# Performance work log

Measured on AMD Instinct MI355X. Metric: run time of the kernel, lower is better.

## Reference

```python
import math
import jax, jax.numpy as jnp
import numpy as np

D_MODEL = 768
N_HEADS = 12


def setup_inputs() -> dict:
    key = jax.random.key(0)
    kx, kw, kb = jax.random.split(key, 3)
    x = jax.random.normal(kx, (2, 2048, D_MODEL), dtype=jnp.float32)
    # nn.Linear(D, 3D): weight [3D, D], bias [3D]; init ~ U(-1/sqrt(D), 1/sqrt(D))
    bound = 1.0 / math.sqrt(D_MODEL)
    W_kqv = jax.random.uniform(kw, (3 * D_MODEL, D_MODEL), dtype=jnp.float32, minval=-bound, maxval=bound)
    b_kqv = jax.random.uniform(kb, (3 * D_MODEL,), dtype=jnp.float32, minval=-bound, maxval=bound)
    return {"x": x, "W_kqv": W_kqv, "b_kqv": b_kqv}


def reference(x, W_kqv, b_kqv):
    N, C, D = x.shape
    H = N_HEADS
    hd = D // H
    z = jnp.einsum('ncd,ed->nce', x, W_kqv) + b_kqv  # [N, C, 3D]
    # order in source: k first, then q, then v
    k = z[:, :, :D].reshape(N, C, H, hd).transpose(0, 2, 1, 3)       # [N,H,C,hd]
    q = z[:, :, D:2 * D].reshape(N, C, H, hd).transpose(0, 2, 1, 3)
    v = z[:, :, 2 * D:].reshape(N, C, H, hd).transpose(0, 2, 1, 3)
    # NOTE: faithful to source: scale by sqrt(D) (full model dim), not sqrt(head_dim)
    scores = jnp.einsum('nhqd,nhkd->nhqk', q, k) / math.sqrt(D)
    causal = jnp.tril(jnp.ones((C, C), dtype=bool))
    scores = jnp.where(causal, scores, -jnp.inf)
    attn = jax.nn.softmax(scores, axis=-1)
    out = jnp.einsum('nhqk,nhkd->nhqd', attn, v)  # [N,H,C,hd]
    return out.transpose(0, 2, 1, 3).reshape(N, C, D)
```

## Files before the change

kernel.cpp:

```cpp
#include <hip/hip_runtime.h>
#include <stdint.h>

#define D_MODEL 768
#define E3      2304
#define NCTX    2048
#define NH      12
#define HD      64
#define MROWS   4096
#define NHTOT   24

typedef __attribute__((ext_vector_type(8))) short short8;
typedef __attribute__((ext_vector_type(4))) short bf16x4;
typedef __attribute__((ext_vector_type(4))) float f32x4;

typedef __attribute__((address_space(3))) uint32_t lds_u32;
typedef __attribute__((address_space(1))) uint32_t glob_u32;

__device__ __forceinline__ void async_copy16(const void* g, void* l) {
    __builtin_amdgcn_global_load_lds((const glob_u32*)(uintptr_t)g,
                                     (lds_u32*)(uint32_t)(uintptr_t)l, 16, 0, 0);
}

__device__ __forceinline__ unsigned short f2bf(float f) {
    uint32_t u = __builtin_bit_cast(uint32_t, f);
    u += 0x7fffu + ((u >> 16) & 1u);
    return (unsigned short)(u >> 16);
}

__device__ __forceinline__ float fast_exp2(float x) {
#if __has_builtin(__builtin_amdgcn_exp2f)
    return __builtin_amdgcn_exp2f(x);
#else
    return __expf(x * 0.6931471805599453f);
#endif
}

#if __has_builtin(__builtin_amdgcn_mfma_f32_16x16x16bf16_1k)
#define HAVE_MFMA16 1
#else
#define HAVE_MFMA16 0
#endif

__global__ void cast_bf16_kernel(const float* __restrict__ in, unsigned short* __restrict__ out) {
    int i = blockIdx.x * blockDim.x + threadIdx.x;
    float4 v = ((const float4*)in)[i];
    ushort4 o;
    o.x = f2bf(v.x); o.y = f2bf(v.y); o.z = f2bf(v.z); o.w = f2bf(v.w);
    ((ushort4*)out)[i] = o;
}

__global__ __launch_bounds__(256) void qkv_gemm(const unsigned short* __restrict__ A,
                                                const unsigned short* __restrict__ B,
                                                const float* __restrict__ bias,
                                                unsigned short* __restrict__ Zq,
                                                unsigned short* __restrict__ Kb,
                                                unsigned short* __restrict__ Vb) {
    __shared__ __attribute__((aligned(16))) unsigned short sA[128 * 64];
    __shared__ __attribute__((aligned(16))) unsigned short sB[128 * 64];

    const int tid  = threadIdx.x;
    const int wave = tid >> 6;
    const int lane = tid & 63;
    const int quad = lane >> 4;
    const int l15  = lane & 15;
    const int wm   = (wave >> 1) << 6;
    const int wn   = (wave & 1) << 6;
    const int row0 = blockIdx.y * 128;
    const int col0 = blockIdx.x * 128;

    const int srow   = lane >> 3;
    const int schunk = (lane & 7) * 8;

    f32x4 acc[4][4] = {};

    for (int k0 = 0; k0 < D_MODEL; k0 += 64) {
        __syncthreads();
#pragma unroll
        for (int c = 0; c < 4; ++c) {
            const int rbase = wave * 32 + c * 8;
            async_copy16(A + (size_t)(row0 + rbase + srow) * D_MODEL + k0 + schunk, &sA[rbase * 64]);
            async_copy16(B + (size_t)(col0 + rbase + srow) * D_MODEL + k0 + schunk, &sB[rbase * 64]);
        }
        __syncthreads();

#pragma unroll
        for (int ks = 0; ks < 2; ++ks) {
            short8 aF[4], bF[4];
#pragma unroll
            for (int i = 0; i < 4; ++i)
                aF[i] = *(const short8*)&sA[(wm + i * 16 + l15) * 64 + ks * 32 + quad * 8];
#pragma unroll
            for (int i = 0; i < 4; ++i)
                bF[i] = *(const short8*)&sB[(wn + i * 16 + l15) * 64 + ks * 32 + quad * 8];
#pragma unroll
            for (int i = 0; i < 4; ++i)
#pragma unroll
                for (int j = 0; j < 4; ++j)
                    acc[i][j] = __builtin_amdgcn_mfma_f32_16x16x32_bf16(aF[i], bF[j], acc[i][j], 0, 0, 0);
        }
    }

    if (col0 < D_MODEL) {
#pragma unroll
        for (int j = 0; j < 4; ++j) {
            const int col = col0 + wn + j * 16 + l15;
            const float bv = bias[col];
            const int h = col >> 6, d = col & 63;
            const int ks = d >> 5, quadd = (d >> 3) & 3, e = d & 7;
#pragma unroll
            for (int i = 0; i < 4; ++i) {
                const int row = row0 + wm + i * 16 + quad * 4;
                const int n = row >> 11;
                const int key = row & (NCTX - 1);
                const int kb = key >> 6;
                const int ct = i;
                const size_t base = ((size_t)((n * NH + h) * 32 + kb)) * 4096
                                  + (((ks * 4 + ct) * 4 + quadd) * 16) * 8 + e;
#pragma unroll
                for (int r = 0; r < 4; ++r)
                    Kb[base + (size_t)(quad * 4 + r) * 8] = f2bf(acc[i][j][r] + bv);
            }
        }
    } else if (col0 < 2 * D_MODEL) {
        const float zscale = 0.036084391824351615f * 1.4426950408889634f;
#pragma unroll
        for (int j = 0; j < 4; ++j) {
            const int col = col0 - D_MODEL + wn + j * 16 + l15;
            const float bv = bias[col0 + wn + j * 16 + l15];
#pragma unroll
            for (int i = 0; i < 4; ++i) {
                const int row = row0 + wm + i * 16 + quad * 4;
#pragma unroll
                for (int r = 0; r < 4; ++r)
                    Zq[(size_t)(row + r) * D_MODEL + col] = f2bf((acc[i][j][r] + bv) * zscale);
            }
        }
    } else {
#pragma unroll
        for (int j = 0; j < 4; ++j) {
            const int col = col0 + wn + j * 16 + l15;
            const float bv = bias[col];
            const int ch = col - 2 * D_MODEL;
            const int h = ch >> 6, d = ch & 63;
            const int dt = d >> 4, l15d = d & 15;
#pragma unroll
            for (int i = 0; i < 4; ++i) {
                const int row = row0 + wm + i * 16 + quad * 4;
                const int n = row >> 11;
                const int key = row & (NCTX - 1);
                const int kb = key >> 6;
                const int ct = i, quadv = quad;
                ushort4 w4;
                w4.x = f2bf(acc[i][j][0] + bv);
                w4.y = f2bf(acc[i][j][1] + bv);
                w4.z = f2bf(acc[i][j][2] + bv);
                w4.w = f2bf(acc[i][j][3] + bv);
                *(ushort4*)&Vb[((size_t)((n * NH + h) * 32 + kb)) * 4096
                               + (((ct * 4 + dt) * 4 + quadv) * 16 + l15d) * 4] = w4;
            }
        }
    }
}

__global__ __launch_bounds__(256) void attn_kernel(const unsigned short* __restrict__ Zq,
                                                   const unsigned short* __restrict__ Kb,
                                                   const unsigned short* __restrict__ Vb,
                                                   float* __restrict__ out) {
    __shared__ __attribute__((aligned(16))) unsigned short sK[2][4096];
    __shared__ __attribute__((aligned(16))) unsigned short sV[2][4096];
#if !HAVE_MFMA16
    __shared__ __attribute__((aligned(16))) unsigned short sP[4][16 * 72];
#endif

    const int tid  = threadIdx.x;
    const int wave = tid >> 6;
    const int lane = tid & 63;
    const int quad = lane >> 4;
    const int l15  = lane & 15;
    const int b    = blockIdx.x;
    const int t    = (NCTX / 64 - 1) - b / NHTOT;
    const int nh   = b - (b / NHTOT) * NHTOT;
    const int n    = nh / NH;
    const int h    = nh - n * NH;

    const unsigned short* KbP = Kb + (size_t)(nh * 32) * 4096;
    const unsigned short* VbP = Vb + (size_t)(nh * 32) * 4096;

    const unsigned short* Qp = Zq + (size_t)(n * NCTX + t * 64 + wave * 16) * D_MODEL + h * HD;
    short8 qf[2];
#pragma unroll
    for (int ks = 0; ks < 2; ++ks)
        qf[ks] = *(const short8*)&Qp[(size_t)l15 * D_MODEL + ks * 32 + quad * 8];

    f32x4 o[4] = {};
    float lsum = 0.0f;

#pragma unroll
    for (int c = 0; c < 2; ++c) {
        const int off = wave * 1024 + c * 512;
        async_copy16(KbP + off + lane * 8, &sK[0][off]);
        async_copy16(VbP + off + lane * 8, &sV[0][off]);
    }

    for (int kb = 0; kb <= t; ++kb) {
        const int buf = kb & 1;
        __syncthreads();
        if (kb < t) {
#pragma unroll
            for (int c = 0; c < 2; ++c) {
                const int off = wave * 1024 + c * 512;
                async_copy16(KbP + (size_t)(kb + 1) * 4096 + off + lane * 8, &sK[buf ^ 1][off]);
                async_copy16(VbP + (size_t)(kb + 1) * 4096 + off + lane * 8, &sV[buf ^ 1][off]);
            }
        }

        short8 kf[2][4];
#pragma unroll
        for (int ks = 0; ks < 2; ++ks)
#pragma unroll
            for (int ct = 0; ct < 4; ++ct)
                kf[ks][ct] = *(const short8*)&sK[buf][(ks * 4 + ct) * 512 + lane * 8];

        f32x4 s[4] = {};
#pragma unroll
        for (int ct = 0; ct < 4; ++ct) {
            s[ct] = __builtin_amdgcn_mfma_f32_16x16x32_bf16(kf[0][ct], qf[0], s[ct], 0, 0, 0);
            s[ct] = __builtin_amdgcn_mfma_f32_16x16x32_bf16(kf[1][ct], qf[1], s[ct], 0, 0, 0);
        }

        const bool diag = (kb == t);
        const int qg = t * 64 + wave * 16 + l15;
#if HAVE_MFMA16
        bf16x4 pA[4];
#endif
#pragma unroll
        for (int ct = 0; ct < 4; ++ct) {
            float pv[4];
#pragma unroll
            for (int r = 0; r < 4; ++r) {
                const int key = kb * 64 + ct * 16 + quad * 4 + r;
                float sv = s[ct][r];
                if (diag && key > qg) sv = -INFINITY;
                pv[r] = fast_exp2(sv);
                lsum += pv[r];
            }
#if HAVE_MFMA16
            pA[ct][0] = (short)f2bf(pv[0]); pA[ct][1] = (short)f2bf(pv[1]);
            pA[ct][2] = (short)f2bf(pv[2]); pA[ct][3] = (short)f2bf(pv[3]);
#else
            ushort4 w4;
            w4.x = f2bf(pv[0]); w4.y = f2bf(pv[1]); w4.z = f2bf(pv[2]); w4.w = f2bf(pv[3]);
            *(ushort4*)&sP[wave][l15 * 72 + ct * 16 + quad * 4] = w4;
#endif
        }

#if HAVE_MFMA16
#pragma unroll
        for (int ct = 0; ct < 4; ++ct)
#pragma unroll
            for (int dt = 0; dt < 4; ++dt) {
                const bf16x4 vf = *(const bf16x4*)&sV[buf][(ct * 4 + dt) * 256 + lane * 4];
                o[dt] = __builtin_amdgcn_mfma_f32_16x16x16bf16_1k(pA[ct], vf, o[dt], 0, 0, 0);
            }
#else
        const short8 pf0 = *(const short8*)&sP[wave][l15 * 72 + quad * 8];
        const short8 pf1 = *(const short8*)&sP[wave][l15 * 72 + 32 + quad * 8];
#pragma unroll
        for (int dt = 0; dt < 4; ++dt) {
            short8 vf0, vf1;
#pragma unroll
            for (int e = 0; e < 8; ++e) {
                const int k0 = quad * 8 + e;
                const int k1 = 32 + quad * 8 + e;
                vf0[e] = (short)sV[buf][(((k0 >> 4) * 4 + dt) * 4 + ((k0 >> 2) & 3)) * 64 + l15 * 4 + (k0 & 3)];
                vf1[e] = (short)sV[buf][(((k1 >> 4) * 4 + dt) * 4 + ((k1 >> 2) & 3)) * 64 + l15 * 4 + (k1 & 3)];
            }
            o[dt] = __builtin_amdgcn_mfma_f32_16x16x32_bf16(pf0, vf0, o[dt], 0, 0, 0);
            o[dt] = __builtin_amdgcn_mfma_f32_16x16x32_bf16(pf1, vf1, o[dt], 0, 0, 0);
        }
#endif
    }

    float l = lsum;
    l += __shfl_xor(l, 16);
    l += __shfl_xor(l, 32);
    const float linv = 1.0f / l;
#pragma unroll
    for (int r = 0; r < 4; ++r) {
        const float inv = __shfl(linv, quad * 4 + r);
        const size_t row = (size_t)n * NCTX + t * 64 + wave * 16 + quad * 4 + r;
#pragma unroll
        for (int dt = 0; dt < 4; ++dt)
            out[row * D_MODEL + h * HD + dt * 16 + l15] = o[dt][r] * inv;
    }
}

extern "C" void kernel_launch(void* const* d_in, const int* in_sizes, int n_in,
                              void* d_out, int out_size, void* d_ws, size_t ws_size,
                              hipStream_t stream) {
    const float* x = (const float*)d_in[0];
    const float* W = (const float*)d_in[1];
    const float* b = (const float*)d_in[2];
    float* out = (float*)d_out;

    unsigned short* xb = (unsigned short*)d_ws;
    unsigned short* Wb = xb + (size_t)MROWS * D_MODEL;
    unsigned short* Zq = Wb + (size_t)E3 * D_MODEL;
    unsigned short* Kb = Zq + (size_t)MROWS * D_MODEL;
    unsigned short* Vb = Kb + (size_t)NHTOT * 32 * 4096;

    cast_bf16_kernel<<<dim3((MROWS * D_MODEL / 4) / 256), 256, 0, stream>>>(x, xb);
    cast_bf16_kernel<<<dim3((E3 * D_MODEL / 4) / 256), 256, 0, stream>>>(W, Wb);
    qkv_gemm<<<dim3(E3 / 128, MROWS / 128), 256, 0, stream>>>(xb, Wb, b, Zq, Kb, Vb);
    attn_kernel<<<dim3(NHTOT * (NCTX / 64)), 256, 0, stream>>>(Zq, Kb, Vb, out);
}
```

Baseline: 146.7 us.

## Triple-buffer attention K/V loads, remap blocks per XCD, merge cast kernels

The attention kernel moves from double to triple buffering of K/V tiles in LDS. It prefetches two tiles ahead and uses explicit vmcnt waits plus a raw barrier instead of __syncthreads, so loads can overlap more compute. Block indices are remapped so that the heads sharing an XCD stay together, meant to improve L2 reuse of K/V, and MFMA sections get raised wave priority. The two fp32-to-bf16 cast launches are merged into one kernel, saving a launch. The cost is 50% more LDS per block, which may lower occupancy, and a hand-coded vmcnt count that must match the number of outstanding loads.

```diff
diff --git a/kernel.cpp b/kernel.cpp
--- a/kernel.cpp
+++ b/kernel.cpp
@@ -41,12 +41,21 @@
 #define HAVE_MFMA16 0
 #endif
 
-__global__ void cast_bf16_kernel(const float* __restrict__ in, unsigned short* __restrict__ out) {
+__global__ __launch_bounds__(256) void cast2_bf16_kernel(const float* __restrict__ a,
+                                                         unsigned short* __restrict__ oa,
+                                                         int na4,
+                                                         const float* __restrict__ b,
+                                                         unsigned short* __restrict__ ob) {
     int i = blockIdx.x * blockDim.x + threadIdx.x;
-    float4 v = ((const float4*)in)[i];
+    const float4* src;
+    ushort4* dst;
+    int idx;
+    if (i < na4) { src = (const float4*)a; dst = (ushort4*)oa; idx = i; }
+    else         { src = (const float4*)b; dst = (ushort4*)ob; idx = i - na4; }
+    float4 v = src[idx];
     ushort4 o;
     o.x = f2bf(v.x); o.y = f2bf(v.y); o.z = f2bf(v.z); o.w = f2bf(v.w);
-    ((ushort4*)out)[i] = o;
+    dst[idx] = o;
 }
 
 __global__ __launch_bounds__(256) void qkv_gemm(const unsigned short* __restrict__ A,
@@ -166,8 +175,8 @@
                                                    const unsigned short* __restrict__ Kb,
                                                    const unsigned short* __restrict__ Vb,
                                                    float* __restrict__ out) {
-    __shared__ __attribute__((aligned(16))) unsigned short sK[2][4096];
-    __shared__ __attribute__((aligned(16))) unsigned short sV[2][4096];
+    __shared__ __attribute__((aligned(16))) unsigned short sK[3][4096];
+    __shared__ __attribute__((aligned(16))) unsigned short sV[3][4096];
 #if !HAVE_MFMA16
     __shared__ __attribute__((aligned(16))) unsigned short sP[4][16 * 72];
 #endif
@@ -178,8 +187,10 @@
     const int quad = lane >> 4;
     const int l15  = lane & 15;
     const int b    = blockIdx.x;
-    const int t    = (NCTX / 64 - 1) - b / NHTOT;
-    const int nh   = b - (b / NHTOT) * NHTOT;
+    const int xcd  = b & 7;
+    const int ii   = b >> 3;
+    const int t    = 31 - ii / 3;
+    const int nh   = (ii % 3) * 8 + xcd;
     const int n    = nh / NH;
     const int h    = nh - n * NH;
 
@@ -195,23 +206,30 @@
     f32x4 o[4] = {};
     float lsum = 0.0f;
 
-#pragma unroll
-    for (int c = 0; c < 2; ++c) {
-        const int off = wave * 1024 + c * 512;
-        async_copy16(KbP + off + lane * 8, &sK[0][off]);
-        async_copy16(VbP + off + lane * 8, &sV[0][off]);
-    }
-
+#define STAGE(kbi, bufi)                                                          \
+    do {                                                                          \
+        const size_t gof = (size_t)(kbi) * 4096;                                  \
+        _Pragma("unroll")                                                         \
+        for (int c = 0; c < 2; ++c) {                                             \
+            const int off = wave * 1024 + c * 512;                                \
+            async_copy16(KbP + gof + off + lane * 8, &sK[bufi][off]);             \
+            async_copy16(VbP + gof + off + lane * 8, &sV[bufi][off]);             \
+        }                                                                         \
+    } while (0)
+
+    STAGE(0, 0);
+    if (t >= 1) STAGE(1, 1);
+
+    int cb = 0;
     for (int kb = 0; kb <= t; ++kb) {
-        const int buf = kb & 1;
-        __syncthreads();
-        if (kb < t) {
-#pragma unroll
-            for (int c = 0; c < 2; ++c) {
-                const int off = wave * 1024 + c * 512;
-                async_copy16(KbP + (size_t)(kb + 1) * 4096 + off + lane * 8, &sK[buf ^ 1][off]);
-                async_copy16(VbP + (size_t)(kb + 1) * 4096 + off + lane * 8, &sV[buf ^ 1][off]);
-            }
+        if (kb == t) { asm volatile("s_waitcnt vmcnt(0)" ::: "memory"); }
+        else         { asm volatile("s_waitcnt vmcnt(4)" ::: "memory"); }
+        __builtin_amdgcn_s_barrier();
+        __builtin_amdgcn_sched_barrier(0);
+
+        if (kb + 2 <= t) {
+            int nb = cb + 2; if (nb >= 3) nb -= 3;
+            STAGE(kb + 2, nb);
         }
 
         short8 kf[2][4];
@@ -219,14 +237,16 @@
         for (int ks = 0; ks < 2; ++ks)
 #pragma unroll
             for (int ct = 0; ct < 4; ++ct)
-                kf[ks][ct] = *(const short8*)&sK[buf][(ks * 4 + ct) * 512 + lane * 8];
+                kf[ks][ct] = *(const short8*)&sK[cb][(ks * 4 + ct) * 512 + lane * 8];
 
         f32x4 s[4] = {};
+        __builtin_amdgcn_s_setprio(1);
 #pragma unroll
         for (int ct = 0; ct < 4; ++ct) {
             s[ct] = __builtin_amdgcn_mfma_f32_16x16x32_bf16(kf[0][ct], qf[0], s[ct], 0, 0, 0);
             s[ct] = __builtin_amdgcn_mfma_f32_16x16x32_bf16(kf[1][ct], qf[1], s[ct], 0, 0, 0);
         }
+        __builtin_amdgcn_s_setprio(0);
 
         const bool diag = (kb == t);
         const int qg = t * 64 + wave * 16 + l15;
@@ -255,13 +275,15 @@
         }
 
 #if HAVE_MFMA16
+        __builtin_amdgcn_s_setprio(1);
 #pragma unroll
         for (int ct = 0; ct < 4; ++ct)
 #pragma unroll
             for (int dt = 0; dt < 4; ++dt) {
-                const bf16x4 vf = *(const bf16x4*)&sV[buf][(ct * 4 + dt) * 256 + lane * 4];
+                const bf16x4 vf = *(const bf16x4*)&sV[cb][(ct * 4 + dt) * 256 + lane * 4];
                 o[dt] = __builtin_amdgcn_mfma_f32_16x16x16bf16_1k(pA[ct], vf, o[dt], 0, 0, 0);
             }
+        __builtin_amdgcn_s_setprio(0);
 #else
         const short8 pf0 = *(const short8*)&sP[wave][l15 * 72 + quad * 8];
         const short8 pf1 = *(const short8*)&sP[wave][l15 * 72 + 32 + quad * 8];
@@ -272,14 +294,16 @@
             for (int e = 0; e < 8; ++e) {
                 const int k0 = quad * 8 + e;
                 const int k1 = 32 + quad * 8 + e;
-                vf0[e] = (short)sV[buf][(((k0 >> 4) * 4 + dt) * 4 + ((k0 >> 2) & 3)) * 64 + l15 * 4 + (k0 & 3)];
-                vf1[e] = (short)sV[buf][(((k1 >> 4) * 4 + dt) * 4 + ((k1 >> 2) & 3)) * 64 + l15 * 4 + (k1 & 3)];
+                vf0[e] = (short)sV[cb][(((k0 >> 4) * 4 + dt) * 4 + ((k0 >> 2) & 3)) * 64 + l15 * 4 + (k0 & 3)];
+                vf1[e] = (short)sV[cb][(((k1 >> 4) * 4 + dt) * 4 + ((k1 >> 2) & 3)) * 64 + l15 * 4 + (k1 & 3)];
             }
             o[dt] = __builtin_amdgcn_mfma_f32_16x16x32_bf16(pf0, vf0, o[dt], 0, 0, 0);
             o[dt] = __builtin_amdgcn_mfma_f32_16x16x32_bf16(pf1, vf1, o[dt], 0, 0, 0);
         }
 #endif
+        cb = (cb + 1 == 3) ? 0 : cb + 1;
     }
+#undef STAGE
 
     float l = lsum;
     l += __shfl_xor(l, 16);
@@ -309,8 +333,9 @@
     unsigned short* Kb = Zq + (size_t)MROWS * D_MODEL;
     unsigned short* Vb = Kb + (size_t)NHTOT * 32 * 4096;
 
-    cast_bf16_kernel<<<dim3((MROWS * D_MODEL / 4) / 256), 256, 0, stream>>>(x, xb);
-    cast_bf16_kernel<<<dim3((E3 * D_MODEL / 4) / 256), 256, 0, stream>>>(W, Wb);
+    const int NA4 = MROWS * D_MODEL / 4;
+    const int NW4 = E3 * D_MODEL / 4;
+    cast2_bf16_kernel<<<dim3((NA4 + NW4) / 256), 256, 0, stream>>>(x, xb, NA4, W, Wb);
     qkv_gemm<<<dim3(E3 / 128, MROWS / 128), 256, 0, stream>>>(xb, Wb, b, Zq, Kb, Vb);
     attn_kernel<<<dim3(NHTOT * (NCTX / 64)), 256, 0, stream>>>(Zq, Kb, Vb, out);
 }
```

Result: slower. 153.1 us (+4.4%).
